# Optimization experiments

Measured on AMD Instinct MI355X. Metric: run time of the kernel, lower is better.

The kernel has to match this reference:

```python
import jax, jax.numpy as jnp
import numpy as np

KNN = 5
SEARCH = 3
CUTOFF = 1.0
NCLASSES = 21
D, H, W = 32, 128, 2048
P = 1048576


def setup_inputs() -> dict:
    key = jax.random.key(0)
    k1, k2, k3, k4, k5, k6 = jax.random.split(key, 6)
    proj_range = jax.random.uniform(k1, (D, H, W), dtype=jnp.float32)
    unproj_range = jax.random.uniform(k2, (P,), dtype=jnp.float32)
    proj_argmax = jax.random.randint(k3, (D, H, W), 0, NCLASSES).astype(jnp.int32)
    px = jax.random.randint(k4, (P,), 0, W).astype(jnp.int32)
    py = jax.random.randint(k5, (P,), 0, H).astype(jnp.int32)
    pz = jax.random.randint(k6, (P,), 0, D).astype(jnp.int32)
    return {"proj_range": proj_range, "unproj_range": unproj_range,
            "proj_argmax": proj_argmax, "px": px, "py": py, "pz": pz}


def reference(proj_range, unproj_range, proj_argmax, px, py, pz):
    pad = (SEARCH - 1) // 2
    k3 = SEARCH ** 3
    center = (k3 - 1) // 2  # = 13 for search=3
    n_pts = unproj_range.shape[0]

    # zero padding replicates F.unfold's implicit zero pad (padded entries stay 0,
    # which is NOT mapped to inf by the `< 0` mask, matching the torch code)
    pr_pad = jnp.pad(proj_range, pad)
    pa_pad = jnp.pad(proj_argmax, pad)

    # kernel offsets, flattened in (dz, dy, dx) order like unfoldNd
    offs = jnp.arange(SEARCH, dtype=jnp.int32)
    oz, oy, ox = jnp.meshgrid(offs, offs, offs, indexing="ij")
    oz, oy, ox = oz.reshape(-1), oy.reshape(-1), ox.reshape(-1)  # [k3]

    # per-point neighborhood indices into the padded volume: [P, k3]
    zi = pz[:, None] + oz[None, :]
    yi = py[:, None] + oy[None, :]
    xi = px[:, None] + ox[None, :]

    nb_rang = pr_pad[zi, yi, xi]                       # [P, k3]
    nb_rang = jnp.where(nb_rang < 0, jnp.inf, nb_rang)
    nb_rang = nb_rang.at[:, center].set(unproj_range)  # center = query range

    k2_dist = jnp.abs(nb_rang - unproj_range[:, None])  # [P, k3]

    neg_top, knn_idx = jax.lax.top_k(-k2_dist, KNN)     # smallest-k distances
    knn_dist = -neg_top                                  # [P, KNN]

    nb_arg = pa_pad[zi, yi, xi]                          # [P, k3] int
    knn_arg = jnp.take_along_axis(nb_arg, knn_idx, axis=1)
    knn_arg = jnp.where(knn_dist > CUTOFF, NCLASSES, knn_arg)  # cutoff -> invalid class

    # scatter-add voting over classes 0..NCLASSES
    counts = jnp.zeros((n_pts, NCLASSES + 1), dtype=proj_range.dtype)
    counts = counts.at[jnp.arange(n_pts, dtype=jnp.int32)[:, None], knn_arg].add(1.0)

    # argmax over classes 1..NCLASSES-1 (drop class 0 and invalid bucket), then +1
    out = jnp.argmax(counts[:, 1:-1], axis=1).astype(jnp.int32) + 1
    return out
```

## Files before the change

### kernel.cpp

```cpp
#include <hip/hip_runtime.h>
#include <math.h>

#define KNN 5
#define K3 27
#define CENTER 13
#define NCLASSES 21
#define DIM_D 32
#define DIM_H 128
#define DIM_W 2048

#define RADIX 256
#define BIN_PTS 2048
#define SEG_TILE 2048


typedef float    float4u __attribute__((ext_vector_type(4), aligned(4)));
typedef int      int4u   __attribute__((ext_vector_type(4), aligned(4)));
typedef unsigned uint2u  __attribute__((ext_vector_type(2), aligned(4)));

#define SENTINEL 3.0e38f
#define BITS_TWO 0x4000000000000000ULL

__device__ __forceinline__ unsigned seg_of_xy(int x, int y) {
    return ((unsigned)y << 1) | ((unsigned)x >> 10);
}
__device__ __forceinline__ unsigned seg_of_wy(unsigned wy) {
    return (((wy >> 11) & 0x7Fu) << 1) | ((wy >> 10) & 1u);
}
__device__ __forceinline__ unsigned b8_of_wy(unsigned wy) {
    return (((wy >> 18) & 31u) << 3) | ((wy >> 7) & 7u);
}

__global__ __launch_bounds__(256) void pack_pa_kernel(
    const int4* __restrict__ pa, uchar4* __restrict__ out, int n4)
{
    int i = blockIdx.x * 256 + threadIdx.x;
    if (i < n4) {
        int4 v = pa[i];
        out[i] = make_uchar4((unsigned char)v.x, (unsigned char)v.y,
                             (unsigned char)v.z, (unsigned char)v.w);
    }
}

__global__ __launch_bounds__(256) void hist0_kernel(
    const int* __restrict__ px, const int* __restrict__ py,
    unsigned* __restrict__ h0, int P)
{
    __shared__ unsigned lh0[RADIX];
    int t = threadIdx.x;
    lh0[t] = 0;
    __syncthreads();
    int base4 = blockIdx.x * 1024 + t;
#pragma unroll
    for (int g = 0; g < 4; ++g) {
        int i4 = base4 + g * 256;
        int i0 = i4 * 4;
        if (i0 + 3 < P) {
            int4 X = ((const int4*)px)[i4];
            int4 Y = ((const int4*)py)[i4];
            atomicAdd(&lh0[seg_of_xy(X.x, Y.x)], 1u);
            atomicAdd(&lh0[seg_of_xy(X.y, Y.y)], 1u);
            atomicAdd(&lh0[seg_of_xy(X.z, Y.z)], 1u);
            atomicAdd(&lh0[seg_of_xy(X.w, Y.w)], 1u);
        } else {
            for (int i = i0; i < P; ++i)
                atomicAdd(&lh0[seg_of_xy(px[i], py[i])], 1u);
        }
    }
    __syncthreads();
    if (lh0[t]) atomicAdd(&h0[t], lh0[t]);
}

__global__ __launch_bounds__(256) void scan256_dup_kernel(
    unsigned* __restrict__ h, unsigned* __restrict__ hbase)
{
    __shared__ unsigned ws[4];
    int t = threadIdx.x, lane = t & 63, wid = t >> 6;
    unsigned a = h[t], ia = a;
#pragma unroll
    for (int off = 1; off < 64; off <<= 1) {
        unsigned v = __shfl_up(ia, off);
        if (lane >= off) ia += v;
    }
    if (lane == 63) ws[wid] = ia;
    __syncthreads();
    unsigned b = 0;
#pragma unroll
    for (int w = 0; w < 4; ++w) b += (w < wid) ? ws[w] : 0u;
    unsigned excl = b + ia - a;
    h[t] = excl;
    hbase[t] = excl;
}

struct BinShared {
    unsigned lh[RADIX];
    unsigned lscan[RADIX];
    unsigned gbase[RADIX];
    unsigned wsum[4];
    unsigned stW[BIN_PTS];
    unsigned stU[BIN_PTS];
    unsigned stI[BIN_PTS];
};

__global__ __launch_bounds__(512) void bin_pass1_kernel(
    const float* __restrict__ ur, const int* __restrict__ px,
    const int* __restrict__ py, const int* __restrict__ pz,
    unsigned* __restrict__ g0,
    unsigned* __restrict__ oW, unsigned* __restrict__ oU,
    unsigned* __restrict__ oI, int P)
{
    __shared__ BinShared S;
    int t = threadIdx.x, lane = t & 63, wid = t >> 6;
    int bstart = blockIdx.x * BIN_PTS;
    int n = min(BIN_PTS, P - bstart);
    if (t < RADIX) S.lh[t] = 0;
    __syncthreads();

    unsigned pw[4], pu[4], rk[4], dg[4];
    {
        int i4 = (bstart >> 2) + t;
        int i0 = i4 * 4;
        if (i0 + 3 < P) {
            int4 X = ((const int4*)px)[i4];
            int4 Y = ((const int4*)py)[i4];
            int4 Z = ((const int4*)pz)[i4];
            float4 U = ((const float4*)ur)[i4];
            int xs[4] = {X.x, X.y, X.z, X.w};
            int ys[4] = {Y.x, Y.y, Y.z, Y.w};
            int zs[4] = {Z.x, Z.y, Z.z, Z.w};
            float us[4] = {U.x, U.y, U.z, U.w};
#pragma unroll
            for (int c = 0; c < 4; ++c) {
                dg[c] = seg_of_xy(xs[c], ys[c]);
                rk[c] = atomicAdd(&S.lh[dg[c]], 1u);
                pw[c] = (unsigned)xs[c] | ((unsigned)ys[c] << 11)
                        | ((unsigned)zs[c] << 18);
                pu[c] = __float_as_uint(us[c]);
            }
        } else {
#pragma unroll
            for (int c = 0; c < 4; ++c) {
                int gi = i0 + c;
                if (gi < P) {
                    int x = px[gi], y = py[gi], z = pz[gi];
                    dg[c] = seg_of_xy(x, y);
                    rk[c] = atomicAdd(&S.lh[dg[c]], 1u);
                    pw[c] = (unsigned)x | ((unsigned)y << 11)
                            | ((unsigned)z << 18);
                    pu[c] = __float_as_uint(ur[gi]);
                } else {
                    dg[c] = 0xFFFFFFFFu;
                }
            }
        }
    }
    __syncthreads();

    {
        unsigned c0 = (t < RADIX) ? S.lh[t] : 0u;
        unsigned inc = c0;
#pragma unroll
        for (int off = 1; off < 64; off <<= 1) {
            unsigned v = __shfl_up(inc, off);
            if (lane >= off) inc += v;
        }
        if (t < RADIX && lane == 63) S.wsum[wid] = inc;
        __syncthreads();
        if (t < RADIX) {
            unsigned wb = 0;
#pragma unroll
            for (int w = 0; w < 4; ++w) wb += (w < wid) ? S.wsum[w] : 0u;
            S.lscan[t] = wb + inc - c0;
            S.gbase[t] = c0 ? atomicAdd(&g0[t], c0) : 0u;
        }
    }
    __syncthreads();
    {
        int i0 = bstart + t * 4 - t * 3;
        (void)i0;
    }
#pragma unroll
    for (int c = 0; c < 4; ++c)
        if (dg[c] != 0xFFFFFFFFu) {
            unsigned sl = S.lscan[dg[c]] + rk[c];
            S.stW[sl] = pw[c];
            S.stU[sl] = pu[c];
            S.stI[sl] = (unsigned)(((bstart >> 2) + t) * 4 + c);
        }
    __syncthreads();
#pragma unroll
    for (int j = 0; j < 4; ++j) {
        int s = j * 512 + t;
        if (s < n) {
            unsigned wv = S.stW[s];
            unsigned d = seg_of_wy(wv);
            unsigned pos = S.gbase[d] + ((unsigned)s - S.lscan[d]);
            oW[pos] = wv;
            oU[pos] = S.stU[s];
            oI[pos] = S.stI[s];
        }
    }
}

__global__ __launch_bounds__(1024) void pass2b_kernel(
    const unsigned* __restrict__ iW, const unsigned* __restrict__ iU,
    const unsigned* __restrict__ iI, const unsigned* __restrict__ segBase,
    unsigned* __restrict__ oW, unsigned* __restrict__ oU,
    unsigned* __restrict__ oI, int P)
{
    __shared__ unsigned bh[RADIX];
    __shared__ unsigned cur[RADIX];
    __shared__ unsigned lz[RADIX];
    __shared__ unsigned lsc[RADIX];
    __shared__ unsigned wsum[4];
    __shared__ unsigned stW[SEG_TILE];
    __shared__ unsigned stU[SEG_TILE];
    __shared__ unsigned stI[SEG_TILE];

    int b = blockIdx.x;
    unsigned s0 = segBase[b];
    unsigned s1 = (b == RADIX - 1) ? (unsigned)P : segBase[b + 1];
    int t = threadIdx.x, lane = t & 63, wid = t >> 6;

    if (t < RADIX) bh[t] = 0;
    __syncthreads();

    for (unsigned i = s0 + t; i < s1; i += 1024)
        atomicAdd(&bh[b8_of_wy(iW[i])], 1u);
    __syncthreads();

    {
        unsigned c0 = (t < RADIX) ? bh[t] : 0u;
        unsigned inc = c0;
#pragma unroll
        for (int off = 1; off < 64; off <<= 1) {
            unsigned v = __shfl_up(inc, off);
            if (lane >= off) inc += v;
        }
        if (t < RADIX && lane == 63) wsum[wid] = inc;
        __syncthreads();
        if (t < RADIX) {
            unsigned wb = 0;
#pragma unroll
            for (int w = 0; w < 4; ++w) wb += (w < wid) ? wsum[w] : 0u;
            cur[t] = s0 + wb + inc - c0;
        }
    }
    __syncthreads();

    for (unsigned tb = s0; tb < s1; tb += SEG_TILE) {
        unsigned m = min((unsigned)SEG_TILE, s1 - tb);
        if (t < RADIX) lz[t] = 0;
        __syncthreads();
        unsigned vw[2], vu[2], vi[2], rk[2], zz[2];
#pragma unroll
        for (int j = 0; j < 2; ++j) {
            int s = j * 1024 + t;
            if (s < (int)m) {
                unsigned gi = tb + (unsigned)s;
                vw[j] = iW[gi];
                vu[j] = iU[gi];
                vi[j] = iI[gi];
                zz[j] = b8_of_wy(vw[j]);
                rk[j] = atomicAdd(&lz[zz[j]], 1u);
            } else {
                zz[j] = 0xFFFFFFFFu;
            }
        }
        __syncthreads();
        {
            unsigned c0 = (t < RADIX) ? lz[t] : 0u;
            unsigned inc = c0;
#pragma unroll
            for (int off = 1; off < 64; off <<= 1) {
                unsigned v = __shfl_up(inc, off);
                if (lane >= off) inc += v;
            }
            if (t < RADIX && lane == 63) wsum[wid] = inc;
            __syncthreads();
            if (t < RADIX) {
                unsigned wb = 0;
#pragma unroll
                for (int w = 0; w < 4; ++w) wb += (w < wid) ? wsum[w] : 0u;
                lsc[t] = wb + inc - c0;
            }
        }
        __syncthreads();
#pragma unroll
        for (int j = 0; j < 2; ++j)
            if (zz[j] != 0xFFFFFFFFu) {
                unsigned sl = lsc[zz[j]] + rk[j];
                stW[sl] = vw[j];
                stU[sl] = vu[j];
                stI[sl] = vi[j];
            }
        __syncthreads();
#pragma unroll
        for (int j = 0; j < 2; ++j) {
            int s = j * 1024 + t;
            if (s < (int)m) {
                unsigned wv = stW[s];
                unsigned d = b8_of_wy(wv);
                unsigned pos = cur[d] + ((unsigned)s - lsc[d]);
                oW[pos] = wv;
                oU[pos] = stU[s];
                oI[pos] = stI[s];
            }
        }
        __syncthreads();
        if (t < RADIX) cur[t] += lz[t];
        __syncthreads();
    }
}

template <bool U8>
__device__ __forceinline__ void bev_knn_body(
    const float* __restrict__ pr, const int* __restrict__ pa,
    const unsigned char* __restrict__ pa8,
    float u, int x, int y, int z, int oidx, int* __restrict__ out)
{
    int xo = min(max(x - 1, 0), DIM_W - 4);
    int s = x - 1 - xo;
    int xo8 = (max(x - 1, 0)) & ~3;
    int sb = (x - 1) - xo8;

    float4u L[9];
    int4u   A[9];
    uint2u  B[9];
    bool okr[9];
#pragma unroll
    for (int r = 0; r < 9; ++r) {
        const int dz = r / 3 - 1;
        const int dy = r % 3 - 1;
        int zz = z + dz, yy = y + dy;
        bool ok = ((unsigned)zz < (unsigned)DIM_D) &
                  ((unsigned)yy < (unsigned)DIM_H);
        okr[r] = ok;
        int row = ok ? (zz * DIM_H + yy) : 0;
        size_t rb = ((size_t)row) << 11;
        L[r] = *(const float4u*)(pr + rb + xo);
        if (U8) B[r] = *(const uint2u*)(pa8 + rb + xo8);
        else    A[r] = *(const int4u*)(pa + rb + xo);
    }

    double bd[KNN];
#pragma unroll
    for (int j = 0; j < KNN; ++j) bd[j] = 1.0e308;

    auto push = [&](int k, float v, unsigned cls) {
        float d = fabsf(v - u);
        d = (v < 0.f) ? SENTINEL : d;
        if (k == CENTER) d = 0.0f;
        double key = (double)d + 1.0;
        unsigned long long kb =
            (unsigned long long)__double_as_longlong(key)
            | (unsigned long long)(((unsigned)k << 5) | (cls & 31u));
        double kd = __longlong_as_double((long long)kb);
#pragma unroll
        for (int j = 0; j < KNN; ++j) {
            double lo = fmin(bd[j], kd);
            kd = fmax(bd[j], kd);
            bd[j] = lo;
        }
    };

    bool fast = __all(s == 0);
    if (fast) {
#pragma unroll
        for (int r = 0; r < 9; ++r) {
            bool ok = okr[r];
            float v0, v1, v2;
            unsigned cc0, cc1, cc2;
            v0 = ok ? L[r].x : 0.f;
            v1 = ok ? L[r].y : 0.f;
            v2 = ok ? L[r].z : 0.f;
            if (U8) {
                unsigned long long v64 =
                    ((unsigned long long)B[r].y << 32) | B[r].x;
                unsigned c3 = ok ? (unsigned)(v64 >> (8 * sb)) : 0u;
                cc0 = c3 & 0xFFu;
                cc1 = (c3 >> 8) & 0xFFu;
                cc2 = (c3 >> 16) & 0xFFu;
            } else {
                cc0 = ok ? (unsigned)A[r].x : 0u;
                cc1 = ok ? (unsigned)A[r].y : 0u;
                cc2 = ok ? (unsigned)A[r].z : 0u;
            }
            push(r * 3 + 0, v0, cc0);
            push(r * 3 + 1, v1, cc1);
            push(r * 3 + 2, v2, cc2);
        }
    } else {
#pragma unroll
        for (int r = 0; r < 9; ++r) {
            bool ok = okr[r];
            float a0 = ok ? L[r].x : 0.f;
            float a1 = ok ? L[r].y : 0.f;
            float a2 = ok ? L[r].z : 0.f;
            float a3 = ok ? L[r].w : 0.f;
            float v0 = (s == 0) ? a0 : ((s == -1) ? 0.f : ((s == 1) ? a1 : a2));
            float v1 = (s == 0) ? a1 : ((s == -1) ? a0 : ((s == 1) ? a2 : a3));
            float v2 = (s == 0) ? a2 : ((s == -1) ? a1 : ((s == 1) ? a3 : 0.f));
            unsigned cv[3];
            if (U8) {
                unsigned long long v64 = ok ?
                    (((unsigned long long)B[r].y << 32) | B[r].x) : 0ULL;
#pragma unroll
                for (int j = 0; j < 3; ++j) {
                    int xm = x - 1 + j;
                    bool xv = (unsigned)xm < (unsigned)DIM_W;
                    int idx = sb + j;
                    idx = idx < 0 ? 0 : idx;
                    unsigned byte = (unsigned)((v64 >> (8 * idx)) & 0xFFu);
                    cv[j] = xv ? byte : 0u;
                }
            } else {
                unsigned c0 = ok ? (unsigned)A[r].x : 0u;
                unsigned c1 = ok ? (unsigned)A[r].y : 0u;
                unsigned c2 = ok ? (unsigned)A[r].z : 0u;
                unsigned c3 = ok ? (unsigned)A[r].w : 0u;
                cv[0] = (s == 0) ? c0 : ((s == -1) ? 0u : ((s == 1) ? c1 : c2));
                cv[1] = (s == 0) ? c1 : ((s == -1) ? c0 : ((s == 1) ? c2 : c3));
                cv[2] = (s == 0) ? c2 : ((s == -1) ? c1 : ((s == 1) ? c3 : 0u));
            }
            push(r * 3 + 0, v0, cv[0]);
            push(r * 3 + 1, v1, cv[1]);
            push(r * 3 + 2, v2, cv[2]);
        }
    }

    int votes[KNN];
#pragma unroll
    for (int j = 0; j < KNN; ++j) {
        unsigned long long kb =
            (unsigned long long)__double_as_longlong(bd[j]);
        int cls = (int)(kb & 31u);
        bool cut = (kb & ~1023ULL) > BITS_TWO;
        votes[j] = cut ? NCLASSES : cls;
    }

    int best_cnt = 0, best_cls = 1;
#pragma unroll
    for (int j = 0; j < KNN; ++j) {
        int v = votes[j];
        if (v >= 1 && v <= NCLASSES - 1) {
            int cnt = 0;
#pragma unroll
            for (int i = 0; i < KNN; ++i) cnt += (votes[i] == v) ? 1 : 0;
            if (cnt > best_cnt || (cnt == best_cnt && v < best_cls)) {
                best_cnt = cnt;
                best_cls = v;
            }
        }
    }
    __builtin_nontemporal_store(best_cls, &out[oidx]);
}

__device__ __forceinline__ int swizzle_block(int b, int nb) {
    if ((nb & 7) == 0) {
        int per = nb >> 3;
        return (b & 7) * per + (b >> 3);
    }
    return b;
}

template <bool U8>
__global__ __launch_bounds__(256) void bev_knn_aos_kernel(
    const float* __restrict__ pr, const int* __restrict__ pa,
    const unsigned char* __restrict__ pa8,
    const unsigned* __restrict__ pW, const unsigned* __restrict__ pU,
    const unsigned* __restrict__ pI, int* __restrict__ out, int P)
{
    int lb = swizzle_block(blockIdx.x, gridDim.x);
    int p = lb * blockDim.x + threadIdx.x;
    if (p >= P) return;
    unsigned wv = __builtin_nontemporal_load(pW + p);
    unsigned uv = __builtin_nontemporal_load(pU + p);
    unsigned iv = __builtin_nontemporal_load(pI + p);
    float u = __uint_as_float(uv);
    int x = (int)(wv & 0x7FFu);
    int y = (int)((wv >> 11) & 0x7Fu);
    int z = (int)((wv >> 18) & 0x1Fu);
    bev_knn_body<U8>(pr, pa, pa8, u, x, y, z, (int)iv, out);
}

__global__ __launch_bounds__(256) void bev_knn_direct_kernel(
    const float* __restrict__ pr, const int* __restrict__ pa,
    const float* __restrict__ ur, const int* __restrict__ px,
    const int* __restrict__ py, const int* __restrict__ pz,
    int* __restrict__ out, int P)
{
    int p = blockIdx.x * blockDim.x + threadIdx.x;
    if (p >= P) return;
    bev_knn_body<false>(pr, pa, (const unsigned char*)nullptr,
                        ur[p], px[p], py[p], pz[p], p, out);
}

extern "C" void kernel_launch(void* const* d_in, const int* in_sizes, int n_in,
                              void* d_out, int out_size, void* d_ws, size_t ws_size,
                              hipStream_t stream) {
    const float* pr = (const float*)d_in[0];
    const float* ur = (const float*)d_in[1];
    const int*   pa = (const int*)d_in[2];
    const int*   px = (const int*)d_in[3];
    const int*   py = (const int*)d_in[4];
    const int*   pz = (const int*)d_in[5];
    int* out = (int*)d_out;
    int P = in_sizes[1];
    int gridH = (P + 4095) / 4096;
    int gridB = (P + BIN_PTS - 1) / BIN_PTS;
    int gridD = (P + 255) / 256;

    const int VOXELS = DIM_D * DIM_H * DIM_W;
    size_t h_b    = (size_t)RADIX * 4;
    size_t hb_b   = (size_t)RADIX * 4;
    size_t pre    = (h_b + hb_b + 255) & ~(size_t)255;
    size_t arr_b  = ((size_t)P * 4 + 255) & ~(size_t)255;
    size_t need   = pre + 6 * arr_b;
    size_t pack_b = ((size_t)VOXELS + 31) & ~(size_t)31;
    size_t need8  = need + pack_b;

    if (ws_size >= need) {
        char* ws = (char*)d_ws;
        unsigned* h0cur  = (unsigned*)ws;
        unsigned* h0base = (unsigned*)(ws + h_b);
        unsigned* p1W = (unsigned*)(ws + pre);
        unsigned* p1U = (unsigned*)(ws + pre + arr_b);
        unsigned* p1I = (unsigned*)(ws + pre + 2 * arr_b);
        unsigned* p2W = (unsigned*)(ws + pre + 3 * arr_b);
        unsigned* p2U = (unsigned*)(ws + pre + 4 * arr_b);
        unsigned* p2I = (unsigned*)(ws + pre + 5 * arr_b);
        unsigned char* pa8 = (unsigned char*)(ws + pre + 6 * arr_b);
        bool use8 = (ws_size >= need8);

        hipMemsetAsync(ws, 0, pre, stream);

        if (use8) {
            int n4 = VOXELS / 4;
            pack_pa_kernel<<<(n4 + 255) / 256, 256, 0, stream>>>(
                (const int4*)pa, (uchar4*)pa8, n4);
        }
        hist0_kernel<<<gridH, 256, 0, stream>>>(px, py, h0cur, P);
        scan256_dup_kernel<<<1, 256, 0, stream>>>(h0cur, h0base);
        bin_pass1_kernel<<<gridB, 512, 0, stream>>>(ur, px, py, pz, h0cur,
                                                    p1W, p1U, p1I, P);
        pass2b_kernel<<<RADIX, 1024, 0, stream>>>(p1W, p1U, p1I, h0base,
                                                  p2W, p2U, p2I, P);
        if (use8)
            bev_knn_aos_kernel<true><<<gridD, 256, 0, stream>>>(
                pr, pa, pa8, p2W, p2U, p2I, out, P);
        else
            bev_knn_aos_kernel<false><<<gridD, 256, 0, stream>>>(
                pr, pa, nullptr, p2W, p2U, p2I, out, P);
    } else {
        bev_knn_direct_kernel<<<gridD, 256, 0, stream>>>(pr, pa, ur, px, py,
                                                         pz, out, P);
    }
}
```

Measured before the change: 183.5 us.

## Fuse class packing with histogram and replace global atomics with partial sums

Merges the int-to-byte packing of proj_argmax and the coarse segment histogram into one launch. The first 256 blocks each histogram a chunk of points and write a per-block partial, and a single-block kernel sums those partials and scans them. This drops the workspace memset, one kernel launch and the global atomics. The cost is a serial 256-iteration reduction inside one block and a 256 KB partial buffer.

```diff
diff --git a/kernel.cpp b/kernel.cpp
--- a/kernel.cpp
+++ b/kernel.cpp
@@ -31,52 +31,55 @@
     return (((wy >> 18) & 31u) << 3) | ((wy >> 7) & 7u);
 }
 
-__global__ __launch_bounds__(256) void pack_pa_kernel(
-    const int4* __restrict__ pa, uchar4* __restrict__ out, int n4)
-{
-    int i = blockIdx.x * 256 + threadIdx.x;
+__global__ __launch_bounds__(256) void pack_hist_kernel(
+    const int4* __restrict__ pa, uchar4* __restrict__ pa8,
+    const int* __restrict__ px, const int* __restrict__ py,
+    unsigned* __restrict__ partial, int n4, int P, int chunk)
+{
+    __shared__ unsigned lh0[RADIX];
+    int t = threadIdx.x, b = blockIdx.x;
+
+    int i = b * 256 + t;
     if (i < n4) {
         int4 v = pa[i];
-        out[i] = make_uchar4((unsigned char)v.x, (unsigned char)v.y,
+        pa8[i] = make_uchar4((unsigned char)v.x, (unsigned char)v.y,
                              (unsigned char)v.z, (unsigned char)v.w);
     }
-}
-
-__global__ __launch_bounds__(256) void hist0_kernel(
-    const int* __restrict__ px, const int* __restrict__ py,
-    unsigned* __restrict__ h0, int P)
-{
-    __shared__ unsigned lh0[RADIX];
-    int t = threadIdx.x;
-    lh0[t] = 0;
-    __syncthreads();
-    int base4 = blockIdx.x * 1024 + t;
-#pragma unroll
-    for (int g = 0; g < 4; ++g) {
-        int i4 = base4 + g * 256;
-        int i0 = i4 * 4;
-        if (i0 + 3 < P) {
-            int4 X = ((const int4*)px)[i4];
-            int4 Y = ((const int4*)py)[i4];
-            atomicAdd(&lh0[seg_of_xy(X.x, Y.x)], 1u);
-            atomicAdd(&lh0[seg_of_xy(X.y, Y.y)], 1u);
-            atomicAdd(&lh0[seg_of_xy(X.z, Y.z)], 1u);
-            atomicAdd(&lh0[seg_of_xy(X.w, Y.w)], 1u);
-        } else {
-            for (int i = i0; i < P; ++i)
-                atomicAdd(&lh0[seg_of_xy(px[i], py[i])], 1u);
-        }
-    }
-    __syncthreads();
-    if (lh0[t]) atomicAdd(&h0[t], lh0[t]);
-}
-
-__global__ __launch_bounds__(256) void scan256_dup_kernel(
-    unsigned* __restrict__ h, unsigned* __restrict__ hbase)
+
+    if (b < RADIX) {
+        lh0[t] = 0;
+        __syncthreads();
+        int start = b * chunk;
+        int end = min(P, start + chunk);
+        for (int i0 = start + t * 4; i0 < end; i0 += 256 * 4) {
+            if (i0 + 3 < end) {
+                int i4 = i0 >> 2;
+                int4 X = ((const int4*)px)[i4];
+                int4 Y = ((const int4*)py)[i4];
+                atomicAdd(&lh0[seg_of_xy(X.x, Y.x)], 1u);
+                atomicAdd(&lh0[seg_of_xy(X.y, Y.y)], 1u);
+                atomicAdd(&lh0[seg_of_xy(X.z, Y.z)], 1u);
+                atomicAdd(&lh0[seg_of_xy(X.w, Y.w)], 1u);
+            } else {
+                for (int j = i0; j < end; ++j)
+                    atomicAdd(&lh0[seg_of_xy(px[j], py[j])], 1u);
+            }
+        }
+        __syncthreads();
+        partial[b * RADIX + t] = lh0[t];
+    }
+}
+
+__global__ __launch_bounds__(256) void scan_reduce_kernel(
+    const unsigned* __restrict__ partial, unsigned* __restrict__ g0,
+    unsigned* __restrict__ hbase)
 {
     __shared__ unsigned ws[4];
     int t = threadIdx.x, lane = t & 63, wid = t >> 6;
-    unsigned a = h[t], ia = a;
+    unsigned a = 0;
+    for (int b = 0; b < RADIX; ++b)
+        a += partial[b * RADIX + t];
+    unsigned ia = a;
 #pragma unroll
     for (int off = 1; off < 64; off <<= 1) {
         unsigned v = __shfl_up(ia, off);
@@ -88,7 +91,7 @@
 #pragma unroll
     for (int w = 0; w < 4; ++w) b += (w < wid) ? ws[w] : 0u;
     unsigned excl = b + ia - a;
-    h[t] = excl;
+    g0[t] = excl;
     hbase[t] = excl;
 }
 
@@ -175,10 +178,6 @@
         }
     }
     __syncthreads();
-    {
-        int i0 = bstart + t * 4 - t * 3;
-        (void)i0;
-    }
 #pragma unroll
     for (int c = 0; c < 4; ++c)
         if (dg[c] != 0xFFFFFFFFu) {
@@ -507,14 +506,15 @@
     const int*   pz = (const int*)d_in[5];
     int* out = (int*)d_out;
     int P = in_sizes[1];
-    int gridH = (P + 4095) / 4096;
     int gridB = (P + BIN_PTS - 1) / BIN_PTS;
     int gridD = (P + 255) / 256;
+    int chunk = (((P + RADIX - 1) / RADIX) + 3) & ~3;
 
     const int VOXELS = DIM_D * DIM_H * DIM_W;
-    size_t h_b    = (size_t)RADIX * 4;
+    size_t g0_b   = (size_t)RADIX * 4;
     size_t hb_b   = (size_t)RADIX * 4;
-    size_t pre    = (h_b + hb_b + 255) & ~(size_t)255;
+    size_t part_b = (size_t)RADIX * RADIX * 4;
+    size_t pre    = (g0_b + hb_b + part_b + 255) & ~(size_t)255;
     size_t arr_b  = ((size_t)P * 4 + 255) & ~(size_t)255;
     size_t need   = pre + 6 * arr_b;
     size_t pack_b = ((size_t)VOXELS + 31) & ~(size_t)31;
@@ -522,8 +522,9 @@
 
     if (ws_size >= need) {
         char* ws = (char*)d_ws;
-        unsigned* h0cur  = (unsigned*)ws;
-        unsigned* h0base = (unsigned*)(ws + h_b);
+        unsigned* g0     = (unsigned*)ws;
+        unsigned* h0base = (unsigned*)(ws + g0_b);
+        unsigned* part   = (unsigned*)(ws + g0_b + hb_b);
         unsigned* p1W = (unsigned*)(ws + pre);
         unsigned* p1U = (unsigned*)(ws + pre + arr_b);
         unsigned* p1I = (unsigned*)(ws + pre + 2 * arr_b);
@@ -533,16 +534,13 @@
         unsigned char* pa8 = (unsigned char*)(ws + pre + 6 * arr_b);
         bool use8 = (ws_size >= need8);
 
-        hipMemsetAsync(ws, 0, pre, stream);
-
-        if (use8) {
-            int n4 = VOXELS / 4;
-            pack_pa_kernel<<<(n4 + 255) / 256, 256, 0, stream>>>(
-                (const int4*)pa, (uchar4*)pa8, n4);
-        }
-        hist0_kernel<<<gridH, 256, 0, stream>>>(px, py, h0cur, P);
-        scan256_dup_kernel<<<1, 256, 0, stream>>>(h0cur, h0base);
-        bin_pass1_kernel<<<gridB, 512, 0, stream>>>(ur, px, py, pz, h0cur,
+        int n4 = use8 ? (VOXELS / 4) : 0;
+        int packBlocks = use8 ? (n4 + 255) / 256 : 0;
+        int gridP = max(packBlocks, RADIX);
+        pack_hist_kernel<<<gridP, 256, 0, stream>>>(
+            (const int4*)pa, (uchar4*)pa8, px, py, part, n4, P, chunk);
+        scan_reduce_kernel<<<1, 256, 0, stream>>>(part, g0, h0base);
+        bin_pass1_kernel<<<gridB, 512, 0, stream>>>(ur, px, py, pz, g0,
                                                     p1W, p1U, p1I, P);
         pass2b_kernel<<<RADIX, 1024, 0, stream>>>(p1W, p1U, p1I, h0base,
                                                   p2W, p2U, p2I, P);
```

After: 182.3 us. Within noise of the previous version (-0.6%).
